# Performance work log

Hardware: AMD Instinct MI355X
Metric: run time of the kernel (lower is better)

The kernel has to match this reference:

```python
import jax, jax.numpy as jnp
import numpy as np

B = 32768
IN_DIM = 1024
HID = 64
COMM = 256          # comm_dim == proto_latent_dim (num_simultaneous_tokens=1)
K = 8192            # num_protos
BETA = 0.25
KL_WEIGHT = 1.0


def setup_inputs() -> dict:
    key = jax.random.key(0)
    ks = jax.random.split(key, 16)
    def lin(kw, fan_in, shape):
        bound = 1.0 / np.sqrt(fan_in)
        return jax.random.uniform(kw, shape, jnp.float32, -bound, bound)
    return {
        "x": jax.random.normal(ks[0], (B, IN_DIM), jnp.float32),
        "eps": jax.random.normal(ks[1], (B, COMM), jnp.float32),
        "W_feat": lin(ks[2], IN_DIM, (IN_DIM, HID)),
        "b_feat": lin(ks[3], IN_DIM, (HID,)),
        "W0": lin(ks[4], HID, (HID, HID)),
        "b0": lin(ks[5], HID, (HID,)),
        "W1": lin(ks[6], HID, (HID, COMM)),
        "b1": lin(ks[7], HID, (COMM,)),
        "W_mu": lin(ks[8], COMM, (COMM, COMM)),
        "b_mu": lin(ks[9], COMM, (COMM,)),
        "W_var": lin(ks[10], COMM, (COMM, COMM)),
        "b_var": lin(ks[11], COMM, (COMM,)),
        "protos": jax.random.uniform(ks[12], (K, COMM), jnp.float32, -1.0 / K, 1.0 / K),
    }


def reference(x, eps, W_feat, b_feat, W0, b0, W1, b1, W_mu, b_mu, W_var, b_var, protos):
    # feature embedder + MLP (num_layers=2, relu after each)
    h = x @ W_feat + b_feat                       # [B, 64]
    h = jax.nn.relu(h @ W0 + b0)                  # [B, 64]
    h = jax.nn.relu(h @ W1 + b1)                  # [B, 256]
    # variational head
    mu = h @ W_mu + b_mu                          # [B, 256]
    logvar = h @ W_var + b_var                    # [B, 256]
    sample = mu + eps * jnp.exp(0.5 * logvar)     # reparameterize
    # VQ layer: pairwise sq-distances to codebook, argmin, gather
    d = (jnp.sum(sample * sample, axis=1, keepdims=True)
         + jnp.sum(protos * protos, axis=1)
         - 2.0 * (sample @ protos.T))             # [B, K]
    idx = jnp.argmin(d, axis=1)                   # [B]
    q = jnp.take(protos, idx, axis=0)             # [B, 256] == one_hot @ protos
    commitment = jnp.mean((jax.lax.stop_gradient(q) - sample) ** 2)
    embedding = jnp.mean((q - jax.lax.stop_gradient(sample)) ** 2)
    vq_loss = BETA * commitment + embedding
    q_st = sample + jax.lax.stop_gradient(q - sample)  # straight-through
    # KL to standard normal
    kld = jnp.mean(-0.5 * jnp.sum(1.0 + logvar - mu * mu - jnp.exp(logvar), axis=1))
    total_loss = KL_WEIGHT * kld + vq_loss
    return q_st, total_loss, kld
```

## Files before the change

### kernel.cpp

```cpp
#include <hip/hip_runtime.h>
#include <cfloat>

#define B_SZ   32768
#define IN_D   1024
#define HID    64
#define COMM   256
#define NPROTO 8192

#define SSCALE 12.0f
#define PSCALE 1.0e6f

typedef __attribute__((ext_vector_type(8))) short bf16x8;
typedef __attribute__((ext_vector_type(4))) float f32x4;
typedef __attribute__((ext_vector_type(4))) int   i32x4;

#define AS1 __attribute__((address_space(1)))
#define AS3 __attribute__((address_space(3)))

__device__ __forceinline__ unsigned short f2bf(float f) {
    unsigned u = __float_as_uint(f);
    unsigned r = u + 0x7fff + ((u >> 16) & 1);
    return (unsigned short)(r >> 16);
}

__device__ __forceinline__ int f2i8(float f, float scale) {
    float v = fminf(fmaxf(f * scale, -127.f), 127.f);
    return __float2int_rn(v);
}

__global__ __launch_bounds__(256) void prep_all(
    const float* __restrict__ Wf,  const float* __restrict__ W0,
    const float* __restrict__ W1,  const float* __restrict__ Wmu,
    const float* __restrict__ Wvar, const float* __restrict__ protos,
    unsigned short* __restrict__ Wft, unsigned short* __restrict__ W0t,
    unsigned short* __restrict__ W1t, unsigned short* __restrict__ Wmt,
    unsigned short* __restrict__ Wvt,
    float* __restrict__ pnormS, char* __restrict__ protoq)
{
    int bid = blockIdx.x;
    if (bid < 848) {
        int gid = bid * 256 + threadIdx.x;
        const float* src; unsigned short* dst; int off, K, N;
        if (gid < 65536)       { src = Wf;  dst = Wft; off = gid;          K = 1024; N = 64;  }
        else if (gid < 69632)  { src = W0;  dst = W0t; off = gid - 65536;  K = 64;   N = 64;  }
        else if (gid < 86016)  { src = W1;  dst = W1t; off = gid - 69632;  K = 64;   N = 256; }
        else if (gid < 151552) { src = Wmu; dst = Wmt; off = gid - 86016;  K = 256;  N = 256; }
        else                   { src = Wvar;dst = Wvt; off = gid - 151552; K = 256;  N = 256; }
        int k = off / N, n = off % N;
        dst[(size_t)n * K + k] = f2bf(src[off]);
    } else {
        int g    = (bid - 848) * 256 + threadIdx.x;
        int p    = g >> 6;
        int lane = g & 63;
        float4 v = *(const float4*)&protos[(size_t)p * COMM + lane * 4];
        int b0 = f2i8(v.x, PSCALE) & 0xff;
        int b1 = f2i8(v.y, PSCALE) & 0xff;
        int b2 = f2i8(v.z, PSCALE) & 0xff;
        int b3 = f2i8(v.w, PSCALE) & 0xff;
        int pk = b0 | (b1 << 8) | (b2 << 16) | (b3 << 24);
        int T = p >> 7, jc = lane >> 2;
        *(int*)(protoq + ((size_t)(T * 16 + jc) * 128 + (p & 127)) * 16 + (lane & 3) * 4) = pk;
        float s = v.x * v.x + v.y * v.y + v.z * v.z + v.w * v.w;
#pragma unroll
        for (int off = 32; off; off >>= 1) s += __shfl_down(s, off);
        if (lane == 0) pnormS[p] = s * (SSCALE * PSCALE);
    }
}

__global__ __launch_bounds__(256, 4) void mlp_fused(
    const float* __restrict__ x,
    const unsigned short* __restrict__ Wft, const float* __restrict__ b_feat,
    const unsigned short* __restrict__ W0t, const float* __restrict__ b0,
    const unsigned short* __restrict__ W1t, const float* __restrict__ b1,
    unsigned short* __restrict__ h3b)
{
    __shared__ __align__(16) char lds[40960];
    char* Xs0 = lds;
    char* Xs1 = lds + 8192;
    char* Ws0 = lds + 16384;
    char* Ws1 = lds + 24576;
    char* H1  = lds + 32768;
    char* H2  = lds + 36864;

    const int t   = threadIdx.x;
    const int w   = t >> 6;
    const int l   = t & 63;
    const int q   = l >> 4;
    const int j16 = l & 15;
    const int rh  = w >> 1;
    const int ch  = w & 1;
    const int rowBase = blockIdx.x * 32;
    const int m = rh * 16 + j16;

    auto stageX = [&](int ks, char* dst) {
#pragma unroll
        for (int i = 0; i < 2; ++i) {
            int p  = i * 256 + t;
            int r  = p >> 4;
            int cs = p & 15;
            int j  = cs ^ (r & 15);
            const float* g = x + (size_t)(rowBase + r) * IN_D + ks * 64 + j * 4;
            void* d = dst + (size_t)(i * 256 + w * 64) * 16;
            __builtin_amdgcn_global_load_lds((const AS1 void*)g, (AS3 void*)d, 16, 0, 0);
        }
    };
    auto stageW = [&](const unsigned short* Wt, int ldk, int ks, char* dst) {
#pragma unroll
        for (int i = 0; i < 2; ++i) {
            int p  = i * 256 + t;
            int n  = p >> 3;
            int cs = p & 7;
            int j  = cs ^ (n & 7);
            const unsigned short* g = Wt + (size_t)n * ldk + ks * 64 + j * 8;
            void* d = dst + (size_t)(i * 256 + w * 64) * 16;
            __builtin_amdgcn_global_load_lds((const AS1 void*)g, (AS3 void*)d, 16, 0, 0);
        }
    };
    auto afragX = [&](const char* Xsb, int kk) -> bf16x8 {
        int jc = kk * 8 + q * 2;
        f32x4 a0 = *(const f32x4*)(Xsb + (size_t)(m * 16 + (jc ^ (m & 15))) * 16);
        f32x4 a1 = *(const f32x4*)(Xsb + (size_t)(m * 16 + ((jc + 1) ^ (m & 15))) * 16);
        bf16x8 o;
        o[0] = (short)f2bf(a0[0]); o[1] = (short)f2bf(a0[1]);
        o[2] = (short)f2bf(a0[2]); o[3] = (short)f2bf(a0[3]);
        o[4] = (short)f2bf(a1[0]); o[5] = (short)f2bf(a1[1]);
        o[6] = (short)f2bf(a1[2]); o[7] = (short)f2bf(a1[3]);
        return o;
    };
    auto bfrag = [&](const char* Wsb, int kk, int v) -> bf16x8 {
        int n  = ch * 32 + 16 * v + j16;
        int jc = kk * 4 + q;
        return *(const bf16x8*)(Wsb + (size_t)(n * 8 + (jc ^ (n & 7))) * 16);
    };
    auto afragH = [&](const char* Hs, int kk) -> bf16x8 {
        int jc = kk * 4 + q;
        return *(const bf16x8*)(Hs + (size_t)(m * 8 + (jc ^ (m & 7))) * 16);
    };

    f32x4 acc1[2];
#pragma unroll
    for (int v = 0; v < 2; ++v) acc1[v] = (f32x4){0.f, 0.f, 0.f, 0.f};

    stageX(0, Xs0);
    stageW(Wft, IN_D, 0, Ws0);
    for (int ks = 0; ks < 16; ++ks) {
        int buf = ks & 1;
        __syncthreads();
        if (ks < 15) {
            stageX(ks + 1, buf ? Xs0 : Xs1);
            stageW(Wft, IN_D, ks + 1, buf ? Ws0 : Ws1);
        }
        const char* Xsb = buf ? Xs1 : Xs0;
        const char* Wsb = buf ? Ws1 : Ws0;
#pragma unroll
        for (int kk = 0; kk < 2; ++kk) {
            bf16x8 af = afragX(Xsb, kk);
#pragma unroll
            for (int v = 0; v < 2; ++v)
                acc1[v] = __builtin_amdgcn_mfma_f32_16x16x32_bf16(
                    af, bfrag(Wsb, kk, v), acc1[v], 0, 0, 0);
        }
    }
#pragma unroll
    for (int v = 0; v < 2; ++v) {
        int c = ch * 32 + 16 * v + j16;
        float bb = b_feat[c];
#pragma unroll
        for (int rg = 0; rg < 4; ++rg) {
            int r = rh * 16 + q * 4 + rg;
            float h = acc1[v][rg] + bb;
            *(short*)(H1 + (size_t)(r * 8 + ((c >> 3) ^ (r & 7))) * 16 + (c & 7) * 2)
                = (short)f2bf(h);
        }
    }
    stageW(W0t, 64, 0, Ws0);
    __syncthreads();

    f32x4 acc2[2];
#pragma unroll
    for (int v = 0; v < 2; ++v) acc2[v] = (f32x4){0.f, 0.f, 0.f, 0.f};
#pragma unroll
    for (int kk = 0; kk < 2; ++kk) {
        bf16x8 af = afragH(H1, kk);
#pragma unroll
        for (int v = 0; v < 2; ++v)
            acc2[v] = __builtin_amdgcn_mfma_f32_16x16x32_bf16(
                af, bfrag(Ws0, kk, v), acc2[v], 0, 0, 0);
    }
#pragma unroll
    for (int v = 0; v < 2; ++v) {
        int c = ch * 32 + 16 * v + j16;
        float bb = b0[c];
#pragma unroll
        for (int rg = 0; rg < 4; ++rg) {
            int r = rh * 16 + q * 4 + rg;
            float h = fmaxf(acc2[v][rg] + bb, 0.f);
            *(short*)(H2 + (size_t)(r * 8 + ((c >> 3) ^ (r & 7))) * 16 + (c & 7) * 2)
                = (short)f2bf(h);
        }
    }
    stageW(W1t, 64, 0, Ws1);
    __syncthreads();

    auto stage3 = [&](int c4, const char* Wsb) {
        f32x4 acc[2];
#pragma unroll
        for (int v = 0; v < 2; ++v) acc[v] = (f32x4){0.f, 0.f, 0.f, 0.f};
#pragma unroll
        for (int kk = 0; kk < 2; ++kk) {
            bf16x8 af = afragH(H2, kk);
#pragma unroll
            for (int v = 0; v < 2; ++v)
                acc[v] = __builtin_amdgcn_mfma_f32_16x16x32_bf16(
                    af, bfrag(Wsb, kk, v), acc[v], 0, 0, 0);
        }
#pragma unroll
        for (int v = 0; v < 2; ++v) {
            int col = c4 * 64 + ch * 32 + 16 * v + j16;
            float bb = b1[col];
#pragma unroll
            for (int rg = 0; rg < 4; ++rg) {
                int row = rowBase + rh * 16 + q * 4 + rg;
                float h = fmaxf(acc[v][rg] + bb, 0.f);
                h3b[(size_t)row * COMM + col] = f2bf(h);
            }
        }
    };
    stageW(W1t + (size_t)64 * 64, 64, 0, Ws0);
    stage3(0, Ws1);
    __syncthreads();
    stageW(W1t + (size_t)128 * 64, 64, 0, Ws1);
    stage3(1, Ws0);
    __syncthreads();
    stageW(W1t + (size_t)192 * 64, 64, 0, Ws0);
    stage3(2, Ws1);
    __syncthreads();
    stage3(3, Ws0);
}

__global__ __launch_bounds__(256, 4) void head_mfma(
    const unsigned short* __restrict__ h3b,
    const unsigned short* __restrict__ Wmt, const float* __restrict__ bmu,
    const unsigned short* __restrict__ Wvt, const float* __restrict__ bvar,
    const float* __restrict__ eps,
    float* __restrict__ sample,
    char* __restrict__ sampleq,
    float* __restrict__ klpart)
{
    __shared__ __align__(16) char lds[32768];
    char* H3 = lds;
    char* Wm = lds + 16384;
    char* Wv = lds + 24576;

    const int t   = threadIdx.x;
    const int w   = t >> 6;
    const int l   = t & 63;
    const int q   = l >> 4;
    const int j16 = l & 15;
    const int rh  = w >> 1;
    const int ch  = w & 1;
    const int rowBase = blockIdx.x * 32;
    const int m = rh * 16 + j16;

#pragma unroll
    for (int i = 0; i < 4; ++i) {
        int p  = i * 256 + t;
        int r  = p >> 5;
        int js = p & 31;
        int j  = (js & 24) | ((js & 7) ^ (r & 7));
        const unsigned short* g = h3b + (size_t)(rowBase + r) * COMM + j * 8;
        void* d = H3 + (size_t)(i * 256 + w * 64) * 16;
        __builtin_amdgcn_global_load_lds((const AS1 void*)g, (AS3 void*)d, 16, 0, 0);
    }

    float kl = 0.f;
    for (int c = 0; c < 4; ++c) {
        f32x4 am[2], av[2];
#pragma unroll
        for (int v = 0; v < 2; ++v) {
            am[v] = (f32x4){0.f, 0.f, 0.f, 0.f};
            av[v] = (f32x4){0.f, 0.f, 0.f, 0.f};
        }
        for (int ks = 0; ks < 4; ++ks) {
            __syncthreads();
#pragma unroll
            for (int i = 0; i < 2; ++i) {
                int p  = i * 256 + t;
                int n  = p >> 3;
                int js = p & 7;
                int j  = js ^ (n & 7);
                const unsigned short* gm =
                    Wmt + (size_t)(c * 64 + n) * COMM + ks * 64 + j * 8;
                const unsigned short* gv =
                    Wvt + (size_t)(c * 64 + n) * COMM + ks * 64 + j * 8;
                void* dm = Wm + (size_t)(i * 256 + w * 64) * 16;
                void* dv = Wv + (size_t)(i * 256 + w * 64) * 16;
                __builtin_amdgcn_global_load_lds((const AS1 void*)gm, (AS3 void*)dm, 16, 0, 0);
                __builtin_amdgcn_global_load_lds((const AS1 void*)gv, (AS3 void*)dv, 16, 0, 0);
            }
            __syncthreads();
#pragma unroll
            for (int kk = 0; kk < 2; ++kk) {
                int jwg = ks * 8 + kk * 4 + q;
                bf16x8 af = *(const bf16x8*)(H3 +
                    (size_t)(m * 32 + ((jwg & 24) | ((jwg & 7) ^ (m & 7)))) * 16);
                int jw = kk * 4 + q;
#pragma unroll
                for (int v = 0; v < 2; ++v) {
                    int n = ch * 32 + 16 * v + j16;
                    size_t pos = (size_t)(n * 8 + (jw ^ (n & 7))) * 16;
                    bf16x8 bm = *(const bf16x8*)(Wm + pos);
                    bf16x8 bv = *(const bf16x8*)(Wv + pos);
                    am[v] = __builtin_amdgcn_mfma_f32_16x16x32_bf16(af, bm, am[v], 0, 0, 0);
                    av[v] = __builtin_amdgcn_mfma_f32_16x16x32_bf16(af, bv, av[v], 0, 0, 0);
                }
            }
        }
#pragma unroll
        for (int v = 0; v < 2; ++v) {
            int col = c * 64 + ch * 32 + 16 * v + j16;
            float bm_ = bmu[col];
            float bv_ = bvar[col];
#pragma unroll
            for (int rg = 0; rg < 4; ++rg) {
                int row = rowBase + rh * 16 + q * 4 + rg;
                float mu = am[v][rg] + bm_;
                float lv = av[v][rg] + bv_;
                float e  = expf(0.5f * lv);
                float s  = mu + eps[(size_t)row * COMM + col] * e;
                sample [(size_t)row * COMM + col] = s;
                sampleq[(size_t)row * COMM + col] = (char)f2i8(s, SSCALE);
                kl += 1.f + lv - mu * mu - e * e;
            }
        }
    }
#pragma unroll
    for (int off = 32; off; off >>= 1) kl += __shfl_down(kl, off);
    __shared__ float wsum[4];
    if (l == 0) wsum[w] = kl;
    __syncthreads();
    if (t == 0)
        klpart[blockIdx.x] = wsum[0] + wsum[1] + wsum[2] + wsum[3];
}

#define SPLITS 4
#define SPAN   (NPROTO / SPLITS)
#define NT     (SPAN / 128)

__global__ __launch_bounds__(256, 2) void vq_argmin_i8(
    const char* __restrict__ sampleq,
    const char* __restrict__ protoq,
    const float* __restrict__ pnormS,
    float* __restrict__ minval,
    int* __restrict__ minidx)
{
    __shared__ __align__(16) char As[32768];
    __shared__ __align__(16) char Bs[2][8192];

    const int t   = threadIdx.x;
    const int w   = t >> 6;
    const int l   = t & 63;
    const int q   = l >> 4;
    const int j16 = l & 15;
    const int wrow = (w >> 1) * 64;
    const int wcol = (w & 1) * 64;
    const int rowBase = blockIdx.x * 128;
    const int tBase   = blockIdx.y * NT;

#pragma unroll
    for (int i = 0; i < 8; ++i) {
        int p  = i * 256 + t;
        int r  = p >> 4;
        int cs = p & 15;
        int j  = cs ^ (r & 15);
        const char* g = sampleq + (size_t)(rowBase + r) * COMM + j * 16;
        void* d = As + (size_t)(i * 256 + w * 64) * 16;
        __builtin_amdgcn_global_load_lds((const AS1 void*)g, (AS3 void*)d, 16, 0, 0);
    }
    {
        const char* src = protoq + (size_t)tBase * 32768;
#pragma unroll
        for (int i = 0; i < 2; ++i) {
            int p = i * 256 + t;
            __builtin_amdgcn_global_load_lds(
                (const AS1 void*)(src + (size_t)p * 16),
                (AS3 void*)(Bs[0] + (size_t)(i * 256 + w * 64) * 16), 16, 0, 0);
        }
    }
    __syncthreads();

    i32x4 af[4][4];
#pragma unroll
    for (int u = 0; u < 4; ++u)
#pragma unroll
        for (int ks = 0; ks < 4; ++ks) {
            int mm = wrow + 16 * u + j16;
            int jc = ks * 4 + q;
            af[u][ks] = *(const i32x4*)(As + (size_t)(mm * 16 + (jc ^ (mm & 15))) * 16);
        }

    float bestv[16];
    int   besti[16];
#pragma unroll
    for (int s = 0; s < 16; ++s) { bestv[s] = FLT_MAX; besti[s] = 0; }

    int buf = 0;
    for (int pt = 0; pt < NT; ++pt) {
        i32x4 acc[4][4];
#pragma unroll
        for (int u = 0; u < 4; ++u)
#pragma unroll
            for (int v = 0; v < 4; ++v) acc[u][v] = (i32x4){0, 0, 0, 0};

        for (int ks = 0; ks < 4; ++ks) {
            if (pt | ks) __syncthreads();
            int nks = ks + 1, npt = pt;
            if (nks == 4) { nks = 0; ++npt; }
            if (npt < NT) {
                const char* src = protoq + ((size_t)(tBase + npt) * 16 + nks * 4) * 2048;
#pragma unroll
                for (int i = 0; i < 2; ++i) {
                    int p = i * 256 + t;
                    __builtin_amdgcn_global_load_lds(
                        (const AS1 void*)(src + (size_t)p * 16),
                        (AS3 void*)(Bs[buf ^ 1] + (size_t)(i * 256 + w * 64) * 16), 16, 0, 0);
                }
            }
            i32x4 bfv[4];
#pragma unroll
            for (int v = 0; v < 4; ++v) {
                int n = wcol + 16 * v + j16;
                bfv[v] = *(const i32x4*)(Bs[buf] + (size_t)(q * 128 + n) * 16);
            }
#pragma unroll
            for (int u = 0; u < 4; ++u)
#pragma unroll
                for (int v = 0; v < 4; ++v)
                    acc[u][v] = __builtin_amdgcn_mfma_i32_16x16x64_i8(
                        af[u][ks], bfv[v], acc[u][v], 0, 0, 0);
            buf ^= 1;
        }
        int pTile = (tBase + pt) * 128;
#pragma unroll
        for (int v = 0; v < 4; ++v) {
            int col  = pTile + wcol + 16 * v + j16;
            float pn = pnormS[col];
#pragma unroll
            for (int u = 0; u < 4; ++u)
#pragma unroll
                for (int rg = 0; rg < 4; ++rg) {
                    float sc   = pn - 2.f * (float)acc[u][v][rg];
                    int   slot = u * 4 + rg;
                    if (sc < bestv[slot]) { bestv[slot] = sc; besti[slot] = col; }
                }
        }
    }
#pragma unroll
    for (int off = 1; off < 16; off <<= 1) {
#pragma unroll
        for (int s = 0; s < 16; ++s) {
            float ov = __shfl_xor(bestv[s], off);
            int   oi = __shfl_xor(besti[s], off);
            if (ov < bestv[s] || (ov == bestv[s] && oi < besti[s])) {
                bestv[s] = ov; besti[s] = oi;
            }
        }
    }
    __syncthreads();
    float* cv = (float*)Bs;
    int*   ci = ((int*)Bs) + 256;
    if (j16 == 0) {
#pragma unroll
        for (int u = 0; u < 4; ++u)
#pragma unroll
            for (int rg = 0; rg < 4; ++rg) {
                int row = wrow + 16 * u + 4 * q + rg;
                cv[(w & 1) * 128 + row] = bestv[u * 4 + rg];
                ci[(w & 1) * 128 + row] = besti[u * 4 + rg];
            }
    }
    __syncthreads();
    if (t < 128) {
        float v0 = cv[t];       int i0 = ci[t];
        float v1 = cv[128 + t]; int i1 = ci[128 + t];
        if (v1 < v0 || (v1 == v0 && i1 < i0)) { v0 = v1; i0 = i1; }
        minval[(size_t)blockIdx.y * B_SZ + rowBase + t] = v0;
        minidx[(size_t)blockIdx.y * B_SZ + rowBase + t] = i0;
    }
}

__global__ __launch_bounds__(256) void gather_kernel(const float* __restrict__ sample,
                                                     const float* __restrict__ protos,
                                                     const float* __restrict__ minval,
                                                     const int* __restrict__ minidx,
                                                     float* __restrict__ out,
                                                     float* __restrict__ msepart)
{
    int t  = threadIdx.x;
    int rb = blockIdx.x * 8;
    __shared__ int sidx[8];
    if (t < 8) {
        int i = rb + t;
        float bv = minval[i];
        int   bi = minidx[i];
#pragma unroll
        for (int s = 1; s < SPLITS; ++s) {
            float v = minval[(size_t)s * B_SZ + i];
            int   j = minidx[(size_t)s * B_SZ + i];
            if (v < bv || (v == bv && j < bi)) { bv = v; bi = j; }
        }
        sidx[t] = bi;
    }
    __syncthreads();
    float part = 0.f;
#pragma unroll
    for (int u = 0; u < 8; ++u) {
        int i  = rb + u;
        int id = sidx[u];
        float qv = protos[(size_t)id * COMM + t];
        float s  = sample[(size_t)i * COMM + t];
        float d  = qv - s;
        out[(size_t)i * COMM + t] = s + d;
        part += d * d;
    }
#pragma unroll
    for (int off = 32; off; off >>= 1) part += __shfl_down(part, off);
    __shared__ float wsum[4];
    if ((t & 63) == 0) wsum[t >> 6] = part;
    __syncthreads();
    if (t == 0) msepart[blockIdx.x] = wsum[0] + wsum[1] + wsum[2] + wsum[3];
}

__global__ __launch_bounds__(256) void finalize_kernel(const float* __restrict__ klpart, int nkl,
                                                       const float* __restrict__ msepart, int nmse,
                                                       float* __restrict__ out)
{
    int t = threadIdx.x;
    double kl = 0.0, mse = 0.0;
    for (int i = t; i < nkl;  i += 256) kl  += (double)klpart[i];
    for (int i = t; i < nmse; i += 256) mse += (double)msepart[i];
#pragma unroll
    for (int off = 32; off; off >>= 1) {
        kl  += __shfl_down(kl, off);
        mse += __shfl_down(mse, off);
    }
    __shared__ double skl[4], smse[4];
    if ((t & 63) == 0) { skl[t >> 6] = kl; smse[t >> 6] = mse; }
    __syncthreads();
    if (t == 0) {
        double K  = skl[0] + skl[1] + skl[2] + skl[3];
        double M  = smse[0] + smse[1] + smse[2] + smse[3];
        double kld = -0.5 * K / (double)B_SZ;
        double vq  = 1.25 * M / ((double)B_SZ * (double)COMM);
        out[(size_t)B_SZ * COMM]     = (float)(kld + vq);
        out[(size_t)B_SZ * COMM + 1] = (float)kld;
    }
}

extern "C" void kernel_launch(void* const* d_in, const int* in_sizes, int n_in,
                              void* d_out, int out_size, void* d_ws, size_t ws_size,
                              hipStream_t stream)
{
    const float* x      = (const float*)d_in[0];
    const float* eps    = (const float*)d_in[1];
    const float* W_feat = (const float*)d_in[2];
    const float* b_feat = (const float*)d_in[3];
    const float* W0     = (const float*)d_in[4];
    const float* b0     = (const float*)d_in[5];
    const float* W1     = (const float*)d_in[6];
    const float* b1     = (const float*)d_in[7];
    const float* W_mu   = (const float*)d_in[8];
    const float* b_mu   = (const float*)d_in[9];
    const float* W_var  = (const float*)d_in[10];
    const float* b_var  = (const float*)d_in[11];
    const float* protos = (const float*)d_in[12];
    float* out = (float*)d_out;

    char* wsb = (char*)d_ws;
    size_t off = 0;
    auto alloc = [&](size_t bytes) -> void* {
        void* p = wsb + off;
        off = (off + bytes + 255) & ~(size_t)255;
        return p;
    };
    unsigned short* Wft     = (unsigned short*)alloc((size_t)IN_D * HID * 2);
    unsigned short* W0t     = (unsigned short*)alloc((size_t)HID * HID * 2);
    unsigned short* W1t     = (unsigned short*)alloc((size_t)HID * COMM * 2);
    unsigned short* Wmt     = (unsigned short*)alloc((size_t)COMM * COMM * 2);
    unsigned short* Wvt     = (unsigned short*)alloc((size_t)COMM * COMM * 2);
    unsigned short* h3b     = (unsigned short*)alloc((size_t)B_SZ * COMM * 2);
    float*          sample  = (float*)alloc((size_t)B_SZ * COMM * 4);
    char*           sampleq = (char*) alloc((size_t)B_SZ * COMM);
    char*           protoq  = (char*) alloc((size_t)NPROTO * COMM);
    float*          pnormS  = (float*)alloc((size_t)NPROTO * 4);
    float*          minval  = (float*)alloc((size_t)SPLITS * B_SZ * 4);
    int*            minidx  = (int*)  alloc((size_t)SPLITS * B_SZ * 4);
    float*          klpart  = (float*)alloc(1024 * 4);
    float*          msepart = (float*)alloc(4096 * 4);

    prep_all<<<2896, 256, 0, stream>>>(W_feat, W0, W1, W_mu, W_var, protos,
                                       Wft, W0t, W1t, Wmt, Wvt, pnormS, protoq);
    mlp_fused<<<B_SZ / 32, 256, 0, stream>>>(x, Wft, b_feat, W0t, b0, W1t, b1, h3b);
    head_mfma<<<B_SZ / 32, 256, 0, stream>>>(h3b, Wmt, b_mu, Wvt, b_var, eps,
                                             sample, sampleq, klpart);
    vq_argmin_i8<<<dim3(B_SZ / 128, SPLITS), 256, 0, stream>>>(sampleq, protoq, pnormS,
                                                               minval, minidx);
    gather_kernel<<<B_SZ / 8, 256, 0, stream>>>(sample, protos, minval, minidx,
                                                out, msepart);
    finalize_kernel<<<1, 256, 0, stream>>>(klpart, 1024, msepart, 4096, out);
}
```

Before: 419.1 us.

## Load VQ prototype and head weight fragments directly from global, drop LDS staging

```diff
diff --git a/kernel.cpp b/kernel.cpp
--- a/kernel.cpp
+++ b/kernel.cpp
@@ -38,18 +38,23 @@
     float* __restrict__ pnormS, char* __restrict__ protoq)
 {
     int bid = blockIdx.x;
-    if (bid < 848) {
+    if (bid < 106) {
         int gid = bid * 256 + threadIdx.x;
-        const float* src; unsigned short* dst; int off, K, N;
-        if (gid < 65536)       { src = Wf;  dst = Wft; off = gid;          K = 1024; N = 64;  }
-        else if (gid < 69632)  { src = W0;  dst = W0t; off = gid - 65536;  K = 64;   N = 64;  }
-        else if (gid < 86016)  { src = W1;  dst = W1t; off = gid - 69632;  K = 64;   N = 256; }
-        else if (gid < 151552) { src = Wmu; dst = Wmt; off = gid - 86016;  K = 256;  N = 256; }
-        else                   { src = Wvar;dst = Wvt; off = gid - 151552; K = 256;  N = 256; }
-        int k = off / N, n = off % N;
-        dst[(size_t)n * K + k] = f2bf(src[off]);
+        if (gid >= 27136) return;
+        const float* src; unsigned short* dst; int c, K, N;
+        if (gid < 8192)       { src = Wf;  dst = Wft; c = gid;          K = 1024; N = 64;  }
+        else if (gid < 8704)  { src = W0;  dst = W0t; c = gid - 8192;   K = 64;   N = 64;  }
+        else if (gid < 10752) { src = W1;  dst = W1t; c = gid - 8704;   K = 64;   N = 256; }
+        else if (gid < 18944) { src = Wmu; dst = Wmt; c = gid - 10752;  K = 256;  N = 256; }
+        else                  { src = Wvar;dst = Wvt; c = gid - 18944;  K = 256;  N = 256; }
+        int n  = c % N;
+        int k0 = (c / N) * 8;
+        bf16x8 o;
+#pragma unroll
+        for (int j = 0; j < 8; ++j) o[j] = (short)f2bf(src[(size_t)(k0 + j) * N + n]);
+        *(bf16x8*)(dst + (size_t)n * K + k0) = o;
     } else {
-        int g    = (bid - 848) * 256 + threadIdx.x;
+        int g    = (bid - 106) * 256 + threadIdx.x;
         int p    = g >> 6;
         int lane = g & 63;
         float4 v = *(const float4*)&protos[(size_t)p * COMM + lane * 4];
@@ -140,7 +145,6 @@
     f32x4 acc1[2];
 #pragma unroll
     for (int v = 0; v < 2; ++v) acc1[v] = (f32x4){0.f, 0.f, 0.f, 0.f};
-
     stageX(0, Xs0);
     stageW(Wft, IN_D, 0, Ws0);
     for (int ks = 0; ks < 16; ++ks) {
@@ -247,10 +251,7 @@
     char* __restrict__ sampleq,
     float* __restrict__ klpart)
 {
-    __shared__ __align__(16) char lds[32768];
-    char* H3 = lds;
-    char* Wm = lds + 16384;
-    char* Wv = lds + 24576;
+    __shared__ __align__(16) char H3[16384];
 
     const int t   = threadIdx.x;
     const int w   = t >> 6;
@@ -272,6 +273,7 @@
         void* d = H3 + (size_t)(i * 256 + w * 64) * 16;
         __builtin_amdgcn_global_load_lds((const AS1 void*)g, (AS3 void*)d, 16, 0, 0);
     }
+    __syncthreads();
 
     float kl = 0.f;
     for (int c = 0; c < 4; ++c) {
@@ -281,36 +283,19 @@
             am[v] = (f32x4){0.f, 0.f, 0.f, 0.f};
             av[v] = (f32x4){0.f, 0.f, 0.f, 0.f};
         }
+#pragma unroll 2
         for (int ks = 0; ks < 4; ++ks) {
-            __syncthreads();
-#pragma unroll
-            for (int i = 0; i < 2; ++i) {
-                int p  = i * 256 + t;
-                int n  = p >> 3;
-                int js = p & 7;
-                int j  = js ^ (n & 7);
-                const unsigned short* gm =
-                    Wmt + (size_t)(c * 64 + n) * COMM + ks * 64 + j * 8;
-                const unsigned short* gv =
-                    Wvt + (size_t)(c * 64 + n) * COMM + ks * 64 + j * 8;
-                void* dm = Wm + (size_t)(i * 256 + w * 64) * 16;
-                void* dv = Wv + (size_t)(i * 256 + w * 64) * 16;
-                __builtin_amdgcn_global_load_lds((const AS1 void*)gm, (AS3 void*)dm, 16, 0, 0);
-                __builtin_amdgcn_global_load_lds((const AS1 void*)gv, (AS3 void*)dv, 16, 0, 0);
-            }
-            __syncthreads();
 #pragma unroll
             for (int kk = 0; kk < 2; ++kk) {
                 int jwg = ks * 8 + kk * 4 + q;
                 bf16x8 af = *(const bf16x8*)(H3 +
                     (size_t)(m * 32 + ((jwg & 24) | ((jwg & 7) ^ (m & 7)))) * 16);
-                int jw = kk * 4 + q;
+                int koff = ks * 64 + kk * 32 + q * 8;
 #pragma unroll
                 for (int v = 0; v < 2; ++v) {
-                    int n = ch * 32 + 16 * v + j16;
-                    size_t pos = (size_t)(n * 8 + (jw ^ (n & 7))) * 16;
-                    bf16x8 bm = *(const bf16x8*)(Wm + pos);
-                    bf16x8 bv = *(const bf16x8*)(Wv + pos);
+                    int n = c * 64 + ch * 32 + 16 * v + j16;
+                    bf16x8 bm = *(const bf16x8*)(Wmt + (size_t)n * COMM + koff);
+                    bf16x8 bv = *(const bf16x8*)(Wvt + (size_t)n * COMM + koff);
                     am[v] = __builtin_amdgcn_mfma_f32_16x16x32_bf16(af, bm, am[v], 0, 0, 0);
                     av[v] = __builtin_amdgcn_mfma_f32_16x16x32_bf16(af, bv, av[v], 0, 0, 0);
                 }
@@ -347,7 +332,7 @@
 #define SPAN   (NPROTO / SPLITS)
 #define NT     (SPAN / 128)
 
-__global__ __launch_bounds__(256, 2) void vq_argmin_i8(
+__global__ __launch_bounds__(256, 3) void vq_argmin_i8(
     const char* __restrict__ sampleq,
     const char* __restrict__ protoq,
     const float* __restrict__ pnormS,
@@ -355,7 +340,6 @@
     int* __restrict__ minidx)
 {
     __shared__ __align__(16) char As[32768];
-    __shared__ __align__(16) char Bs[2][8192];
 
     const int t   = threadIdx.x;
     const int w   = t >> 6;
@@ -377,34 +361,20 @@
         void* d = As + (size_t)(i * 256 + w * 64) * 16;
         __builtin_amdgcn_global_load_lds((const AS1 void*)g, (AS3 void*)d, 16, 0, 0);
     }
-    {
-        const char* src = protoq + (size_t)tBase * 32768;
-#pragma unroll
-        for (int i = 0; i < 2; ++i) {
-            int p = i * 256 + t;
-            __builtin_amdgcn_global_load_lds(
-                (const AS1 void*)(src + (size_t)p * 16),
-                (AS3 void*)(Bs[0] + (size_t)(i * 256 + w * 64) * 16), 16, 0, 0);
-        }
-    }
-    __syncthreads();
-
-    i32x4 af[4][4];
-#pragma unroll
-    for (int u = 0; u < 4; ++u)
-#pragma unroll
-        for (int ks = 0; ks < 4; ++ks) {
-            int mm = wrow + 16 * u + j16;
-            int jc = ks * 4 + q;
-            af[u][ks] = *(const i32x4*)(As + (size_t)(mm * 16 + (jc ^ (mm & 15))) * 16);
-        }
+    __syncthreads();
+
+    const char* bbase = protoq + ((size_t)(tBase * 16 + q) * 128 + wcol + j16) * 16;
 
     float bestv[16];
     int   besti[16];
 #pragma unroll
     for (int s = 0; s < 16; ++s) { bestv[s] = FLT_MAX; besti[s] = 0; }
 
-    int buf = 0;
+    i32x4 bfv[4], bnx[4];
+#pragma unroll
+    for (int v = 0; v < 4; ++v)
+        bfv[v] = *(const i32x4*)(bbase + v * 256);
+
     for (int pt = 0; pt < NT; ++pt) {
         i32x4 acc[4][4];
 #pragma unroll
@@ -412,33 +382,30 @@
 #pragma unroll
             for (int v = 0; v < 4; ++v) acc[u][v] = (i32x4){0, 0, 0, 0};
 
+#pragma unroll
         for (int ks = 0; ks < 4; ++ks) {
-            if (pt | ks) __syncthreads();
-            int nks = ks + 1, npt = pt;
-            if (nks == 4) { nks = 0; ++npt; }
-            if (npt < NT) {
-                const char* src = protoq + ((size_t)(tBase + npt) * 16 + nks * 4) * 2048;
-#pragma unroll
-                for (int i = 0; i < 2; ++i) {
-                    int p = i * 256 + t;
-                    __builtin_amdgcn_global_load_lds(
-                        (const AS1 void*)(src + (size_t)p * 16),
-                        (AS3 void*)(Bs[buf ^ 1] + (size_t)(i * 256 + w * 64) * 16), 16, 0, 0);
-                }
-            }
-            i32x4 bfv[4];
-#pragma unroll
-            for (int v = 0; v < 4; ++v) {
-                int n = wcol + 16 * v + j16;
-                bfv[v] = *(const i32x4*)(Bs[buf] + (size_t)(q * 128 + n) * 16);
+            int nid = pt * 4 + ks + 1;
+            if (nid < NT * 4) {
+                const char* nb = bbase + (size_t)nid * 8192;
+#pragma unroll
+                for (int v = 0; v < 4; ++v)
+                    bnx[v] = *(const i32x4*)(nb + v * 256);
+            }
+            i32x4 af[4];
+            int jc = ks * 4 + q;
+#pragma unroll
+            for (int u = 0; u < 4; ++u) {
+                int mm = wrow + 16 * u + j16;
+                af[u] = *(const i32x4*)(As + (size_t)(mm * 16 + (jc ^ (mm & 15))) * 16);
             }
 #pragma unroll
             for (int u = 0; u < 4; ++u)
 #pragma unroll
                 for (int v = 0; v < 4; ++v)
                     acc[u][v] = __builtin_amdgcn_mfma_i32_16x16x64_i8(
-                        af[u][ks], bfv[v], acc[u][v], 0, 0, 0);
-            buf ^= 1;
+                        af[u], bfv[v], acc[u][v], 0, 0, 0);
+#pragma unroll
+            for (int v = 0; v < 4; ++v) bfv[v] = bnx[v];
         }
         int pTile = (tBase + pt) * 128;
 #pragma unroll
@@ -467,8 +434,8 @@
         }
     }
     __syncthreads();
-    float* cv = (float*)Bs;
-    int*   ci = ((int*)Bs) + 256;
+    float* cv = (float*)As;
+    int*   ci = ((int*)As) + 256;
     if (j16 == 0) {
 #pragma unroll
         for (int u = 0; u < 4; ++u)
@@ -598,7 +565,7 @@
     float*          klpart  = (float*)alloc(1024 * 4);
     float*          msepart = (float*)alloc(4096 * 4);
 
-    prep_all<<<2896, 256, 0, stream>>>(W_feat, W0, W1, W_mu, W_var, protos,
+    prep_all<<<2154, 256, 0, stream>>>(W_feat, W0, W1, W_mu, W_var, protos,
                                        Wft, W0t, W1t, Wmt, Wvt, pnormS, protoq);
     mlp_fused<<<B_SZ / 32, 256, 0, stream>>>(x, Wft, b_feat, W0t, b0, W1t, b1, h3b);
     head_mfma<<<B_SZ / 32, 256, 0, stream>>>(h3b, Wmt, b_mu, Wvt, b_var, eps,
```

Result: slower. 550.9 us (+31.5%).
